# Kernel optimization log

Measured on AMD Instinct MI355X. Metric: run time of the kernel, lower is better.

## Reference

```python
import jax, jax.numpy as jnp
import numpy as np

VOCAB = 64
EMBED = 256
HIDDEN = 1024
BATCH = 256
SEQLEN = 512


def setup_inputs() -> dict:
    key = jax.random.key(0)
    ks = jax.random.split(key, 5)
    return {
        "x": jax.random.randint(ks[0], (BATCH, SEQLEN), 0, VOCAB),
        "embedding": jax.random.normal(ks[1], (VOCAB, EMBED), dtype=jnp.float32),
        "W_ih": jax.random.normal(ks[2], (EMBED, HIDDEN), dtype=jnp.float32) * 0.01,
        "W_hh": jax.random.normal(ks[3], (HIDDEN, HIDDEN), dtype=jnp.float32) * 0.01,
        "b_h": jnp.zeros((HIDDEN,), dtype=jnp.float32),
        "W_ho": jax.random.normal(ks[4], (HIDDEN, VOCAB), dtype=jnp.float32) * 0.01,
        "b_o": jnp.zeros((VOCAB,), dtype=jnp.float32),
    }


def reference(x, embedding, W_ih, W_hh, b_h, W_ho, b_o):
    # x: [B, L] int indices
    b, l = x.shape
    x_embed = embedding[x]                 # [B, L, E]
    # Precompute the input projection for all timesteps at once: [L, B, H]
    x_proj = jnp.einsum('ble,eh->lbh', x_embed, W_ih) + b_h
    h0 = jnp.zeros((b, W_hh.shape[0]), dtype=x_embed.dtype)

    def step(h_prev, xp_t):
        h_t = jnp.tanh(xp_t + h_prev @ W_hh)   # [B, H]
        return h_t, h_t

    final_hidden, outputs = jax.lax.scan(step, h0, x_proj)  # outputs: [L, B, H]
    outputs = outputs.transpose(1, 0, 2)                    # [B, L, H]
    logits = outputs @ W_ho + b_o                           # [B, L, V]
    return logits, final_hidden
```

## Files before the change

kernel.cpp:

```cpp
#include <hip/hip_runtime.h>
#include <stdint.h>


#define BATCH 256
#define SEQ   512
#define HID   1024
#define VOC   64
#define EMB   256
#define FINAL_OFF (BATCH * SEQ * VOC)
#define RING_SLOTS 32
#define BH (BATCH * HID)
#define CNT_STRIDE 8448

typedef __attribute__((ext_vector_type(8))) short short8;
typedef __attribute__((ext_vector_type(4))) float f32x4;
typedef unsigned long long u64;

__device__ inline unsigned short f2bf(float f) {
  union { float f; unsigned u; } v; v.f = f;
  unsigned u = v.u;
  return (unsigned short)((u + 0x7FFFu + ((u >> 16) & 1u)) >> 16);
}

__device__ __forceinline__ float ftanh(float v) {
  float e = __expf(2.0f * v);
  return fmaf(-2.0f, __builtin_amdgcn_rcpf(e + 1.0f), 1.0f);
}

__device__ inline u64 cload64(const unsigned short* p) {
  return __hip_atomic_load((const u64*)p, __ATOMIC_RELAXED,
                           __HIP_MEMORY_SCOPE_AGENT);
}
__device__ inline void cstore32(unsigned short* p, unsigned v) {
  __hip_atomic_store((unsigned*)p, v, __ATOMIC_RELAXED,
                     __HIP_MEMORY_SCOPE_AGENT);
}

__global__ __launch_bounds__(256) void k_prep(const float* __restrict__ emb,
                                              const float* __restrict__ Wih,
                                              const float* __restrict__ bh,
                                              float* __restrict__ proj) {
  __shared__ float es[EMB];
  const int v = blockIdx.x >> 2;
  const int p = blockIdx.x & 3;
  const int tid = threadIdx.x;
  es[tid] = emb[v * EMB + tid];
  __syncthreads();
  const int h = p * 256 + tid;
  float acc = bh[h];
  for (int e = 0; e < EMB; ++e) acc += es[e] * Wih[e * HID + h];
  proj[v * HID + h] = acc;
}

__global__ __launch_bounds__(256) void k_prep2(const float* __restrict__ Who,
                                               unsigned short* __restrict__ wof) {
  const int e = blockIdx.x * 256 + threadIdx.x;
  const int l15 = e & 15, vt = (e >> 4) & 3, qq = (e >> 6) & 3, kb = e >> 8;
  #pragma unroll
  for (int j = 0; j < 8; ++j)
    wof[e * 8 + j] = f2bf(Who[(kb * 32 + qq * 8 + j) * VOC + vt * 16 + l15]);
}

__device__ __forceinline__ void barrier_arrive(unsigned int* cnt_i, int tid) {
  __syncthreads();
  if (tid == 0) atomicAdd(cnt_i, 1u);
}
__device__ __forceinline__ void barrier_wait(unsigned int* cnt_i, int tid,
                                             int round) {
  if (tid == 0) {
    int guard = 0;
    while (__hip_atomic_load(cnt_i, __ATOMIC_RELAXED, __HIP_MEMORY_SCOPE_AGENT)
           < 16u * (unsigned)round) {
      __builtin_amdgcn_s_sleep(1);
      if (++guard > (1 << 16)) break;
    }
  }
  __syncthreads();
}

__global__ __launch_bounds__(256, 1) void k_rnn(
    const int* __restrict__ x, const float* __restrict__ Whh,
    const float* __restrict__ proj, const unsigned short* __restrict__ wof,
    const float* __restrict__ bo, unsigned short* __restrict__ ring,
    float* __restrict__ out, float* __restrict__ final_out,
    unsigned int* __restrict__ cnt) {
  extern __shared__ char smem[];
  unsigned short* w_lds = (unsigned short*)smem;
  char*           h_lds = smem;

  const int tid = threadIdx.x, bid = blockIdx.x;
  const int gi = bid & 15, gj = bid >> 4;
  const int row0 = gi * 16;
  const int lane = tid & 63, wv = tid >> 6;
  const int l15 = lane & 15, q = lane >> 4;

  for (int it = 0; it < 256; ++it) {
    int u = it * 256 + tid;
    int k = u >> 6, n = u & 63;
    int kb = k >> 5, qq = (k >> 3) & 3, j8 = k & 7;
    w_lds[(size_t)kb * 2048 + qq * 512 + n * 8 + j8] =
        f2bf(Whh[k * HID + gj * 64 + n]);
  }
  __syncthreads();

  short8 bfr[32];
  {
    const char* bbase = (const char*)w_lds + q * 1024 + (wv * 16 + l15) * 16;
    #pragma unroll
    for (int kb = 0; kb < 32; ++kb)
      bfr[kb] = *(const short8*)(bbase + (size_t)kb * 4096);
  }
  __syncthreads();

  unsigned int* cnt_i = (unsigned int*)((char*)cnt + gi * CNT_STRIDE);

  const int hcol = gj * 64 + wv * 16 + l15;
  const char* abase = h_lds + l15 * 2064 + q * 16;
  const float bias = bo[wv * 16 + l15];
  const char* wofb = (const char*)wof + ((q * 4 + wv) * 16 + l15) * 16;

  for (int t = 0; t < SEQ; ++t) {
    int xv = (lane < 16) ? x[(row0 + lane) * SEQ + t] : 0;
    f32x4 a0 = {0.f, 0.f, 0.f, 0.f}, a1 = {0.f, 0.f, 0.f, 0.f};
    f32x4 a2 = {0.f, 0.f, 0.f, 0.f}, a3 = {0.f, 0.f, 0.f, 0.f};
    if (t > 0) {
      #pragma unroll
      for (int kb = 0; kb < 32; kb += 4) {
        short8 af0 = *(const short8*)(abase + (kb + 0) * 64);
        a0 = __builtin_amdgcn_mfma_f32_16x16x32_bf16(af0, bfr[kb + 0], a0, 0, 0, 0);
        short8 af1 = *(const short8*)(abase + (kb + 1) * 64);
        a1 = __builtin_amdgcn_mfma_f32_16x16x32_bf16(af1, bfr[kb + 1], a1, 0, 0, 0);
        short8 af2 = *(const short8*)(abase + (kb + 2) * 64);
        a2 = __builtin_amdgcn_mfma_f32_16x16x32_bf16(af2, bfr[kb + 2], a2, 0, 0, 0);
        short8 af3 = *(const short8*)(abase + (kb + 3) * 64);
        a3 = __builtin_amdgcn_mfma_f32_16x16x32_bf16(af3, bfr[kb + 3], a3, 0, 0, 0);
      }
    }
    unsigned short* slot = ring + (size_t)(t & (RING_SLOTS - 1)) * BH;
    float hv[4];
    #pragma unroll
    for (int r = 0; r < 4; ++r) {
      int row = q * 4 + r;
      int xi = __shfl(xv, row);
      float av = (a0[r] + a1[r]) + (a2[r] + a3[r]);
      hv[r] = ftanh(proj[(size_t)xi * HID + hcol] + av);
      if (t == SEQ - 1) final_out[(size_t)(row0 + row) * HID + hcol] = hv[r];
    }
    #pragma unroll
    for (int r = 0; r < 4; ++r) {
      unsigned myb = f2bf(hv[r]);
      unsigned oth = (unsigned)__shfl_xor((int)myb, 1);
      if ((l15 & 1) == 0) {
        int b = row0 + q * 4 + r;
        cstore32(slot + (size_t)b * HID + hcol, myb | (oth << 16));
      }
    }
    barrier_arrive(cnt_i, tid);
    if ((t & 15) == 15) {
      int tsel = (t - 16) + gj;
      if (tsel >= 0) {
        const unsigned short* hs =
            ring + (size_t)(tsel & (RING_SLOTS - 1)) * BH +
            (size_t)(row0 + l15) * HID + q * 8;
        f32x4 lc = {0.f, 0.f, 0.f, 0.f};
        for (int g = 0; g < 4; ++g) {
          u64 hb[16];
          #pragma unroll
          for (int j = 0; j < 8; ++j) {
            const unsigned short* pk = hs + (g * 8 + j) * 32;
            hb[2 * j]     = cload64(pk);
            hb[2 * j + 1] = cload64(pk + 4);
          }
          #pragma unroll
          for (int j = 0; j < 8; ++j) {
            union { u64 d[2]; short8 s8; } c;
            c.d[0] = hb[2 * j]; c.d[1] = hb[2 * j + 1];
            short8 w8 = *(const short8*)(wofb + (size_t)(g * 8 + j) * 4096);
            lc = __builtin_amdgcn_mfma_f32_16x16x32_bf16(c.s8, w8, lc, 0, 0, 0);
          }
        }
        #pragma unroll
        for (int rr = 0; rr < 4; ++rr) {
          int b = row0 + q * 4 + rr;
          out[((size_t)b * SEQ + tsel) * VOC + wv * 16 + l15] = lc[rr] + bias;
        }
      }
    }
    barrier_wait(cnt_i, tid, t + 1);
    if (t < SEQ - 1) {
      u64 tmp[16];
      #pragma unroll
      for (int rr = 0; rr < 16; ++rr)
        tmp[rr] = cload64(slot + (size_t)(row0 + rr) * HID + tid * 4);
      #pragma unroll
      for (int rr = 0; rr < 16; ++rr)
        *(u64*)(h_lds + rr * 2064 + tid * 8) = tmp[rr];
      __syncthreads();
    }
  }

  if (gj == 15) {
    int tsel = SEQ - 1;
    const unsigned short* hs =
        ring + (size_t)(tsel & (RING_SLOTS - 1)) * BH +
        (size_t)(row0 + l15) * HID + q * 8;
    f32x4 lc = {0.f, 0.f, 0.f, 0.f};
    for (int g = 0; g < 4; ++g) {
      u64 hb[16];
      #pragma unroll
      for (int j = 0; j < 8; ++j) {
        const unsigned short* pk = hs + (g * 8 + j) * 32;
        hb[2 * j]     = cload64(pk);
        hb[2 * j + 1] = cload64(pk + 4);
      }
      #pragma unroll
      for (int j = 0; j < 8; ++j) {
        union { u64 d[2]; short8 s8; } c;
        c.d[0] = hb[2 * j]; c.d[1] = hb[2 * j + 1];
        short8 w8 = *(const short8*)(wofb + (size_t)(g * 8 + j) * 4096);
        lc = __builtin_amdgcn_mfma_f32_16x16x32_bf16(c.s8, w8, lc, 0, 0, 0);
      }
    }
    #pragma unroll
    for (int rr = 0; rr < 4; ++rr) {
      int b = row0 + q * 4 + rr;
      out[((size_t)b * SEQ + tsel) * VOC + wv * 16 + l15] = lc[rr] + bias;
    }
  }
}

extern "C" void kernel_launch(void* const* d_in, const int* in_sizes, int n_in,
                              void* d_out, int out_size, void* d_ws, size_t ws_size,
                              hipStream_t stream) {
  const int*   x   = (const int*)d_in[0];
  const float* emb = (const float*)d_in[1];
  const float* Wih = (const float*)d_in[2];
  const float* Whh = (const float*)d_in[3];
  const float* bh  = (const float*)d_in[4];
  const float* Who = (const float*)d_in[5];
  const float* bo  = (const float*)d_in[6];
  float* out = (float*)d_out;

  char* ws = (char*)d_ws;
  float*          proj = (float*)ws;
  unsigned int*   cnt  = (unsigned int*)(ws + 262144);
  unsigned short* wof  = (unsigned short*)(ws + 524288);
  unsigned short* ring = (unsigned short*)(ws + (1 << 20));

  size_t need = (size_t)(1 << 20) + (size_t)RING_SLOTS * BATCH * HID * 2;
  if (ws_size < need) return;

  (void)hipFuncSetAttribute(reinterpret_cast<const void*>(k_rnn),
                            hipFuncAttributeMaxDynamicSharedMemorySize, 131072);

  k_prep<<<256, 256, 0, stream>>>(emb, Wih, bh, proj);
  k_prep2<<<32, 256, 0, stream>>>(Who, wof);
  hipMemsetAsync(cnt, 0, 262144, stream);
  k_rnn<<<256, 256, 131072, stream>>>(x, Whh, proj, wof, bo, ring,
                                      out, out + FINAL_OFF, cnt);
}
```

Measured before the change: 1.838 ms.

## Remap RNN blocks by XCC so hidden-state exchange stays in shared L2

At startup each block reads its hardware XCC id and counts arrivals per XCC, so blocks in the same batch row group can be placed on the same XCC. When every XCC holds exactly 32 blocks, the kernel reassigns (gi, gj) by XCC. In that case the ring of hidden states is written with plain stores and read with sc0 loads rather than agent-scope atomics, so the per-step exchange can be served from the local L2 instead of going device-wide. This relies on XCC L2 coherence among blocks that share the same rows. It adds a startup handshake, and if placement is uneven it falls back to the old mapping.

```diff
diff --git a/kernel.cpp b/kernel.cpp
--- a/kernel.cpp
+++ b/kernel.cpp
@@ -35,6 +35,12 @@
   __hip_atomic_store((unsigned*)p, v, __ATOMIC_RELAXED,
                      __HIP_MEMORY_SCOPE_AGENT);
 }
+__device__ __forceinline__ u64 ld64_sc0(const unsigned short* p) {
+  u64 v;
+  asm volatile("global_load_dwordx2 %0, %1, off sc0"
+               : "=v"(v) : "v"(p) : "memory");
+  return v;
+}
 
 __global__ __launch_bounds__(256) void k_prep(const float* __restrict__ emb,
                                               const float* __restrict__ Wih,
@@ -89,10 +95,51 @@
   char*           h_lds = smem;
 
   const int tid = threadIdx.x, bid = blockIdx.x;
-  const int gi = bid & 15, gj = bid >> 4;
-  const int row0 = gi * 16;
   const int lane = tid & 63, wv = tid >> 6;
   const int l15 = lane & 15, q = lane >> 4;
+
+  int* sx = (int*)smem;
+  if (tid == 0) {
+    unsigned xcc;
+    asm volatile("s_getreg_b32 %0, hwreg(HW_REG_XCC_ID)" : "=s"(xcc));
+    xcc &= 7u;
+    unsigned* xreg = cnt + 32768;
+    unsigned* xtot = cnt + 33792;
+    unsigned m = atomicAdd(xreg + xcc * 32, 1u);
+    asm volatile("s_waitcnt vmcnt(0)" ::: "memory");
+    atomicAdd(xtot, 1u);
+    unsigned tot = 0; int guard = 0;
+    do {
+      tot = __hip_atomic_load(xtot, __ATOMIC_RELAXED, __HIP_MEMORY_SCOPE_AGENT);
+      if (tot >= 256u) break;
+      __builtin_amdgcn_s_sleep(2);
+    } while (++guard < (1 << 16));
+    int ok = (tot >= 256u) && (m < 32u);
+    for (int i = 0; i < 8; ++i)
+      ok &= (__hip_atomic_load(xreg + i * 32, __ATOMIC_RELAXED,
+                               __HIP_MEMORY_SCOPE_AGENT) == 32u);
+    if (!ok) atomicAdd(cnt + 33824, 1u);
+    asm volatile("s_waitcnt vmcnt(0)" ::: "memory");
+    atomicAdd(cnt + 33856, 1u);
+    unsigned vt = 0; guard = 0;
+    do {
+      vt = __hip_atomic_load(cnt + 33856, __ATOMIC_RELAXED,
+                             __HIP_MEMORY_SCOPE_AGENT);
+      if (vt >= 256u) break;
+      __builtin_amdgcn_s_sleep(2);
+    } while (++guard < (1 << 16));
+    unsigned vf = __hip_atomic_load(cnt + 33824, __ATOMIC_RELAXED,
+                                    __HIP_MEMORY_SCOPE_AGENT);
+    int mode = (vt >= 256u) && (vf == 0u) && ok;
+    sx[0] = mode;
+    sx[1] = mode ? ((int)xcc * 2 + (int)(m >> 4)) : (bid & 15);
+    sx[2] = mode ? (int)(m & 15) : (bid >> 4);
+  }
+  __syncthreads();
+  const int mode = sx[0];
+  const int gi = sx[1], gj = sx[2];
+  const int row0 = gi * 16;
+  __syncthreads();
 
   for (int it = 0; it < 256; ++it) {
     int u = it * 256 + tid;
@@ -152,7 +199,10 @@
       unsigned oth = (unsigned)__shfl_xor((int)myb, 1);
       if ((l15 & 1) == 0) {
         int b = row0 + q * 4 + r;
-        cstore32(slot + (size_t)b * HID + hcol, myb | (oth << 16));
+        unsigned short* p = slot + (size_t)b * HID + hcol;
+        unsigned pk = myb | (oth << 16);
+        if (mode) *(unsigned*)p = pk;
+        else      cstore32(p, pk);
       }
     }
     barrier_arrive(cnt_i, tid);
@@ -165,11 +215,22 @@
         f32x4 lc = {0.f, 0.f, 0.f, 0.f};
         for (int g = 0; g < 4; ++g) {
           u64 hb[16];
-          #pragma unroll
-          for (int j = 0; j < 8; ++j) {
-            const unsigned short* pk = hs + (g * 8 + j) * 32;
-            hb[2 * j]     = cload64(pk);
-            hb[2 * j + 1] = cload64(pk + 4);
+          if (mode) {
+            #pragma unroll
+            for (int j = 0; j < 8; ++j) {
+              const unsigned short* pk = hs + (g * 8 + j) * 32;
+              hb[2 * j]     = ld64_sc0(pk);
+              hb[2 * j + 1] = ld64_sc0(pk + 4);
+            }
+            asm volatile("s_waitcnt vmcnt(0)" ::: "memory");
+            __builtin_amdgcn_sched_barrier(0);
+          } else {
+            #pragma unroll
+            for (int j = 0; j < 8; ++j) {
+              const unsigned short* pk = hs + (g * 8 + j) * 32;
+              hb[2 * j]     = cload64(pk);
+              hb[2 * j + 1] = cload64(pk + 4);
+            }
           }
           #pragma unroll
           for (int j = 0; j < 8; ++j) {
@@ -189,9 +250,17 @@
     barrier_wait(cnt_i, tid, t + 1);
     if (t < SEQ - 1) {
       u64 tmp[16];
-      #pragma unroll
-      for (int rr = 0; rr < 16; ++rr)
-        tmp[rr] = cload64(slot + (size_t)(row0 + rr) * HID + tid * 4);
+      if (mode) {
+        #pragma unroll
+        for (int rr = 0; rr < 16; ++rr)
+          tmp[rr] = ld64_sc0(slot + (size_t)(row0 + rr) * HID + tid * 4);
+        asm volatile("s_waitcnt vmcnt(0)" ::: "memory");
+        __builtin_amdgcn_sched_barrier(0);
+      } else {
+        #pragma unroll
+        for (int rr = 0; rr < 16; ++rr)
+          tmp[rr] = cload64(slot + (size_t)(row0 + rr) * HID + tid * 4);
+      }
       #pragma unroll
       for (int rr = 0; rr < 16; ++rr)
         *(u64*)(h_lds + rr * 2064 + tid * 8) = tmp[rr];
@@ -207,11 +276,22 @@
     f32x4 lc = {0.f, 0.f, 0.f, 0.f};
     for (int g = 0; g < 4; ++g) {
       u64 hb[16];
-      #pragma unroll
-      for (int j = 0; j < 8; ++j) {
-        const unsigned short* pk = hs + (g * 8 + j) * 32;
-        hb[2 * j]     = cload64(pk);
-        hb[2 * j + 1] = cload64(pk + 4);
+      if (mode) {
+        #pragma unroll
+        for (int j = 0; j < 8; ++j) {
+          const unsigned short* pk = hs + (g * 8 + j) * 32;
+          hb[2 * j]     = ld64_sc0(pk);
+          hb[2 * j + 1] = ld64_sc0(pk + 4);
+        }
+        asm volatile("s_waitcnt vmcnt(0)" ::: "memory");
+        __builtin_amdgcn_sched_barrier(0);
+      } else {
+        #pragma unroll
+        for (int j = 0; j < 8; ++j) {
+          const unsigned short* pk = hs + (g * 8 + j) * 32;
+          hb[2 * j]     = cload64(pk);
+          hb[2 * j + 1] = cload64(pk + 4);
+        }
       }
       #pragma unroll
       for (int j = 0; j < 8; ++j) {
```

New measurement: 2.184 ms. +18.8%, slower.
